# Kernel optimization log

Hardware: AMD Instinct MI355X
Metric: run time of the kernel (lower is better)

Reference implementation:

```python
import jax, jax.numpy as jnp
import numpy as np

B, H, W, D = 8, 128, 128, 256
NHEAD, DK = 8, 32
WS = 8
NH, NW = H // WS, W // WS
SHIFT = WS // 2
SCALE = 1.0 / np.sqrt(DK)
WSQ = WS * WS


def _region_labels(h, w, ws, shift):
    lab = np.zeros((h, w), np.int32)
    cnt = 0
    for hs in (slice(0, h - ws), slice(h - ws, h - shift), slice(h - shift, h)):
        for vs in (slice(0, w - ws), slice(w - ws, w - shift), slice(w - shift, w)):
            lab[hs, vs] = cnt
            cnt += 1
    return np.roll(lab, (-shift, -shift), axis=(0, 1))


def _window_labels(lab, ws, nh, nw):
    return lab.reshape(nh, ws, nw, ws).transpose(0, 2, 1, 3).reshape(nh, nw, ws * ws)


# static Swin attention mask: (nh, nw, WSQ, WSQ) bool, True = masked
_lq = _window_labels(_region_labels(H, W, WS, SHIFT), WS, NH, NW)
_lk = _window_labels(_region_labels(H, W, WS, SHIFT), WS, NH, NW)
MASK = jnp.asarray(_lq[..., :, None] != _lk[..., None, :])

# static relative position index: (WSQ, WSQ) into (2*WS-1)^2 table
_coords = np.stack(np.meshgrid(np.arange(WS), np.arange(WS), indexing='ij'), -1).reshape(-1, 2)
_rel = _coords[:, None, :] - _coords[None, :, :] + (WS - 1)  # in [0, 2*WS-2]
REL_INDEX = jnp.asarray(_rel[..., 0] * (2 * WS - 1) + _rel[..., 1])


def _cyclic_shift(t, s):
    # t: (B, nhead, H, W, d)
    return jnp.roll(t, (-s, -s), axis=(2, 3))


def _partition(t):
    # (B, nhead, H, W, d) -> (B, nhead, NH, NW, WSQ, d)
    b, nh_, _, _, d = t.shape
    t = t.reshape(b, nh_, NH, WS, NW, WS, d)
    return t.transpose(0, 1, 2, 4, 3, 5, 6).reshape(b, nh_, NH, NW, WSQ, d)


def _merge(t):
    # (B, nhead, NH, NW, WSQ, d) -> (B, nhead, H, W, d)
    b, nh_, _, _, _, d = t.shape
    t = t.reshape(b, nh_, NH, NW, WS, WS, d).transpose(0, 1, 2, 4, 3, 5, 6)
    return t.reshape(b, nh_, NH * WS, NW * WS, d)


def setup_inputs() -> dict:
    key = jax.random.key(0)
    ks = jax.random.split(key, 6)
    return {
        'x': jax.random.normal(ks[0], (B, H, W, D), jnp.float32),
        'z': jax.random.normal(ks[1], (B, H, W, D), jnp.float32),
        'Wq': jax.random.normal(ks[2], (D, D), jnp.float32) * 0.02,
        'bq': jnp.zeros((D,), jnp.float32),
        'Wkv': jax.random.normal(ks[3], (D, 2 * D), jnp.float32) * 0.02,
        'bkv': jnp.zeros((2 * D,), jnp.float32),
        'Wo': jax.random.normal(ks[4], (D, D), jnp.float32) * 0.02,
        'bo': jnp.zeros((D,), jnp.float32),
        'rel_table': jax.random.normal(ks[5], ((2 * WS - 1) ** 2, NHEAD), jnp.float32) * 0.02,
    }


def reference(x, z, Wq, bq, Wkv, bkv, Wo, bo, rel_table):
    b = x.shape[0]
    q = (x @ Wq + bq).reshape(b, H, W, NHEAD, DK).transpose(0, 3, 1, 2, 4)
    kv = (z @ Wkv + bkv).reshape(b, H, W, 2, NHEAD, DK).transpose(3, 0, 4, 1, 2, 5)
    k, v = kv[0], kv[1]

    q = _partition(_cyclic_shift(q, SHIFT))
    k = _partition(_cyclic_shift(k, SHIFT))
    v = _partition(_cyclic_shift(v, SHIFT))

    # scores: (B, nhead, NH, NW, WSQ, WSQ)
    scores = jnp.einsum('bhijqd,bhijkd->bhijqk', q, k) * SCALE
    pe = rel_table[REL_INDEX]                       # (WSQ, WSQ, nhead)
    scores = scores + pe.transpose(2, 0, 1)[None, :, None, None]
    scores = jnp.where(MASK, jnp.float32(-1e9), scores)
    attn = jax.nn.softmax(scores, axis=-1)

    out = jnp.einsum('bhijqk,bhijkd->bhijqd', attn, v)
    out = _cyclic_shift(_merge(out), -SHIFT)        # (B, nhead, H, W, DK)
    out = out.transpose(0, 2, 3, 1, 4).reshape(b, H, W, D)
    return out @ Wo + bo
```

## Files before the change

### kernel.cpp

```cpp
#include <hip/hip_runtime.h>
#include <hip/hip_bf16.h>


typedef __bf16  bf16x8 __attribute__((ext_vector_type(8)));
typedef short   short8 __attribute__((ext_vector_type(8)));
typedef short   short4v __attribute__((ext_vector_type(4)));
typedef float   f32x4  __attribute__((ext_vector_type(4)));

#define SCALE_F 0.17677669529663687f

__device__ __forceinline__ short f2bs(float f){
    __hip_bfloat16 h = __float2bfloat16(f);
    return __builtin_bit_cast(short, h);
}
__device__ __forceinline__ short8 cvt8(float4 a, float4 b){
    short8 t;
    t[0]=f2bs(a.x); t[1]=f2bs(a.y); t[2]=f2bs(a.z); t[3]=f2bs(a.w);
    t[4]=f2bs(b.x); t[5]=f2bs(b.y); t[6]=f2bs(b.z); t[7]=f2bs(b.w);
    return t;
}
__device__ __forceinline__ int strip3(int r, int c){
    if (c == 0) return 0;
    if (c == 1) return (r < 4) ? 0 : 1;
    return (r < 4) ? 2 : 0;
}

__global__ __launch_bounds__(256) void prep_k(const float* __restrict__ Wq,
                                              const float* __restrict__ Wkv,
                                              const float* __restrict__ Wo,
                                              const float* __restrict__ rel,
                                              short* __restrict__ Wqt,
                                              short* __restrict__ Wkvt,
                                              short* __restrict__ Wot,
                                              float* __restrict__ ADD){
    int i = blockIdx.x * 256 + threadIdx.x;
    if (i < 65536){
        int n = i >> 8, k = i & 255;
        Wqt[i] = f2bs(Wq[k * 256 + n]);
    } else if (i < 196608){
        int j = i - 65536;
        int n = j >> 8, k = j & 255;
        Wkvt[j] = f2bs(Wkv[k * 512 + n]);
    } else if (i < 262144){
        int j = i - 196608;
        int n = j >> 8, k = j & 255;
        Wot[j] = f2bs(Wo[k * 256 + n]);
    } else {
        int j = i - 262144;
        int k = j & 63, q = (j >> 6) & 63, head = (j >> 12) & 7, cls = j >> 15;
        int wiC = cls / 3, wjC = cls - wiC * 3;
        int qr = q >> 3, qc = q & 7, kr = k >> 3, kc = k & 7;
        int lq = strip3(qr, wiC) * 3 + strip3(qc, wjC);
        int lk = strip3(kr, wiC) * 3 + strip3(kc, wjC);
        float pe = rel[((qr - kr + 7) * 15 + (qc - kc + 7)) * 8 + head];
        ADD[j] = (lq != lk) ? -1e9f : pe;
    }
}

__global__ __launch_bounds__(512, 2) void qkv_k(
    const float* __restrict__ x, const float* __restrict__ z,
    const short* __restrict__ Wqt, const short* __restrict__ Wkvt,
    const float* __restrict__ bq, const float* __restrict__ bkv,
    short* __restrict__ Qw, short* __restrict__ Kw, short* __restrict__ Vw){
    __shared__ __align__(16) short lds[2 * 16896];
    const int tid = threadIdx.x, w = tid >> 6, lane = tid & 63;
    const int l15 = lane & 15, g = lane >> 4;
    const int bx = blockIdx.x;
    const int wj = bx & 15, wi = (bx >> 4) & 15, b = bx >> 8;
    const f32x4 zero = {0.f,0.f,0.f,0.f};

#pragma unroll
    for (int i=0;i<4;++i){
        const int u = tid + i*512;
        const int p = u >> 5, c8 = u & 31;
        const int pr = ((wi << 3) + (p >> 3) + 4) & 127;
        const int pc = ((wj << 3) + (p & 7) + 4) & 127;
        const size_t gidx = ((((((size_t)b << 7) | pr) << 7) | pc) << 8) + c8*8;
        const float4* xp = reinterpret_cast<const float4*>(x + gidx);
        float4 a0 = xp[0], a1 = xp[1];
        *reinterpret_cast<short8*>(lds + p*264 + c8*8) = cvt8(a0, a1);
        const float4* zp = reinterpret_cast<const float4*>(z + gidx);
        float4 b0 = zp[0], b1 = zp[1];
        *reinterpret_cast<short8*>(lds + 16896 + p*264 + c8*8) = cvt8(b0, b1);
    }
    __syncthreads();

    const int c0 = w * 32;
    const size_t base = ((((size_t)b*8 + w)*16 + wi)*16 + wj) * 2048;

    {
        f32x4 acc[4][2];
#pragma unroll
        for (int mi=0;mi<4;++mi){ acc[mi][0]=zero; acc[mi][1]=zero; }
#pragma unroll
        for (int kt=0;kt<8;++kt){
            bf16x8 af[4], wf[2];
#pragma unroll
            for (int nj=0;nj<2;++nj)
                wf[nj] = *reinterpret_cast<const bf16x8*>(Wqt + (size_t)(c0 + nj*16 + l15)*256 + kt*32 + g*8);
#pragma unroll
            for (int mi=0;mi<4;++mi)
                af[mi] = *reinterpret_cast<const bf16x8*>(lds + (mi*16 + l15)*264 + kt*32 + g*8);
#pragma unroll
            for (int mi=0;mi<4;++mi)
#pragma unroll
                for (int nj=0;nj<2;++nj)
                    acc[mi][nj] = __builtin_amdgcn_mfma_f32_16x16x32_bf16(af[mi], wf[nj], acc[mi][nj], 0,0,0);
        }
#pragma unroll
        for (int nj=0;nj<2;++nj){
            float bv = bq[c0 + nj*16 + l15];
#pragma unroll
            for (int mi=0;mi<4;++mi)
#pragma unroll
                for (int r=0;r<4;++r)
                    Qw[base + (size_t)(mi*16 + g*4 + r)*32 + nj*16 + l15] = f2bs(acc[mi][nj][r] + bv);
        }
    }
    {
        f32x4 acc[4][2];
#pragma unroll
        for (int mi=0;mi<4;++mi){ acc[mi][0]=zero; acc[mi][1]=zero; }
#pragma unroll
        for (int kt=0;kt<8;++kt){
            bf16x8 af[4], wf[2];
#pragma unroll
            for (int nj=0;nj<2;++nj)
                wf[nj] = *reinterpret_cast<const bf16x8*>(Wkvt + (size_t)(c0 + nj*16 + l15)*256 + kt*32 + g*8);
#pragma unroll
            for (int mi=0;mi<4;++mi)
                af[mi] = *reinterpret_cast<const bf16x8*>(lds + 16896 + (mi*16 + l15)*264 + kt*32 + g*8);
#pragma unroll
            for (int mi=0;mi<4;++mi)
#pragma unroll
                for (int nj=0;nj<2;++nj)
                    acc[mi][nj] = __builtin_amdgcn_mfma_f32_16x16x32_bf16(af[mi], wf[nj], acc[mi][nj], 0,0,0);
        }
#pragma unroll
        for (int nj=0;nj<2;++nj){
            float bv = bkv[c0 + nj*16 + l15];
#pragma unroll
            for (int mi=0;mi<4;++mi)
#pragma unroll
                for (int r=0;r<4;++r)
                    Kw[base + (size_t)(mi*16 + g*4 + r)*32 + nj*16 + l15] = f2bs(acc[mi][nj][r] + bv);
        }
    }
    {
        f32x4 acc[4][2];
#pragma unroll
        for (int mi=0;mi<4;++mi){ acc[mi][0]=zero; acc[mi][1]=zero; }
#pragma unroll
        for (int kt=0;kt<8;++kt){
            bf16x8 af[4], wf[2];
#pragma unroll
            for (int nj=0;nj<2;++nj)
                wf[nj] = *reinterpret_cast<const bf16x8*>(Wkvt + (size_t)(256 + c0 + nj*16 + l15)*256 + kt*32 + g*8);
#pragma unroll
            for (int mi=0;mi<4;++mi)
                af[mi] = *reinterpret_cast<const bf16x8*>(lds + 16896 + (mi*16 + l15)*264 + kt*32 + g*8);
#pragma unroll
            for (int mi=0;mi<4;++mi)
#pragma unroll
                for (int nj=0;nj<2;++nj)
                    acc[mi][nj] = __builtin_amdgcn_mfma_f32_16x16x32_bf16(af[mi], wf[nj], acc[mi][nj], 0,0,0);
        }
#pragma unroll
        for (int nj=0;nj<2;++nj){
            float bv = bkv[256 + c0 + nj*16 + l15];
            const int dk = nj*16 + l15;
#pragma unroll
            for (int mi=0;mi<4;++mi){
                short4v t;
#pragma unroll
                for (int r=0;r<4;++r) t[r] = f2bs(acc[mi][nj][r] + bv);
                *reinterpret_cast<short4v*>(Vw + base + (size_t)dk*64 + mi*16 + g*4) = t;
            }
        }
    }
}

__global__ __launch_bounds__(256, 2) void attnO_k(
    const short* __restrict__ Qw, const short* __restrict__ Kw,
    const short* __restrict__ Vw, const short* __restrict__ Wot,
    const float* __restrict__ bo, const float* __restrict__ ADD,
    float* __restrict__ out){
    __shared__ __align__(16) short lds[4*4608 + 16896];
    const int tid = threadIdx.x, w = tid >> 6, lane = tid & 63;
    const int l15 = lane & 15, g = lane >> 4;
    const int bx = blockIdx.x;
    const int wj = bx & 15, wi = (bx >> 4) & 15, b = bx >> 8;
    const int wiC = (wi > 13) ? wi - 13 : 0;
    const int wjC = (wj > 13) ? wj - 13 : 0;
    short* P   = lds + w * 4608;
    short* att = lds + 18432;
    const f32x4 zero = {0.f,0.f,0.f,0.f};

    for (int hh = 0; hh < 2; ++hh){
        const int h = w + hh * 4;
        const size_t base = ((((size_t)b*8 + h)*16 + wi)*16 + wj) * 2048;

        bf16x8 aq[4], bk[4];
#pragma unroll
        for (int mi=0;mi<4;++mi)
            aq[mi] = *reinterpret_cast<const bf16x8*>(Qw + base + (size_t)(mi*16 + l15)*32 + g*8);
#pragma unroll
        for (int ni=0;ni<4;++ni)
            bk[ni] = *reinterpret_cast<const bf16x8*>(Kw + base + (size_t)(ni*16 + l15)*32 + g*8);
        f32x4 s[4][4];
#pragma unroll
        for (int mi=0;mi<4;++mi)
#pragma unroll
            for (int ni=0;ni<4;++ni)
                s[mi][ni] = __builtin_amdgcn_mfma_f32_16x16x32_bf16(aq[mi], bk[ni], zero, 0,0,0);

        const float* addb = ADD + (size_t)(((wiC*3 + wjC)*8 + h) << 12);
        float rs[4][4];
#pragma unroll
        for (int mi=0;mi<4;++mi){
            const int qbase = mi*16 + g*4;
#pragma unroll
            for (int ni=0;ni<4;++ni){
                const int k = ni*16 + l15;
#pragma unroll
                for (int r=0;r<4;++r)
                    s[mi][ni][r] = fmaf(s[mi][ni][r], SCALE_F, addb[((qbase + r) << 6) + k]);
            }
#pragma unroll
            for (int r=0;r<4;++r){
                float mx = fmaxf(fmaxf(s[mi][0][r], s[mi][1][r]), fmaxf(s[mi][2][r], s[mi][3][r]));
                mx = fmaxf(mx, __shfl_xor(mx, 1));
                mx = fmaxf(mx, __shfl_xor(mx, 2));
                mx = fmaxf(mx, __shfl_xor(mx, 4));
                mx = fmaxf(mx, __shfl_xor(mx, 8));
                float sum = 0.f;
#pragma unroll
                for (int ni=0;ni<4;++ni){
                    float p = __expf(s[mi][ni][r] - mx);
                    s[mi][ni][r] = p;
                    sum += p;
                }
                sum += __shfl_xor(sum, 1);
                sum += __shfl_xor(sum, 2);
                sum += __shfl_xor(sum, 4);
                sum += __shfl_xor(sum, 8);
                rs[mi][r] = 1.f / sum;
                const int q = qbase + r;
#pragma unroll
                for (int ni=0;ni<4;++ni)
                    P[q*72 + ni*16 + l15] = f2bs(s[mi][ni][r]);
            }
        }

        f32x4 o[4][2];
#pragma unroll
        for (int mi=0;mi<4;++mi){ o[mi][0]=zero; o[mi][1]=zero; }
#pragma unroll
        for (int ks=0;ks<2;++ks){
            bf16x8 pa[4], vb[2];
#pragma unroll
            for (int mi=0;mi<4;++mi)
                pa[mi] = *reinterpret_cast<const bf16x8*>(P + (mi*16 + l15)*72 + ks*32 + g*8);
#pragma unroll
            for (int nj=0;nj<2;++nj)
                vb[nj] = *reinterpret_cast<const bf16x8*>(Vw + base + (size_t)(nj*16 + l15)*64 + ks*32 + g*8);
#pragma unroll
            for (int mi=0;mi<4;++mi)
#pragma unroll
                for (int nj=0;nj<2;++nj)
                    o[mi][nj] = __builtin_amdgcn_mfma_f32_16x16x32_bf16(pa[mi], vb[nj], o[mi][nj], 0,0,0);
        }

#pragma unroll
        for (int mi=0;mi<4;++mi)
#pragma unroll
            for (int nj=0;nj<2;++nj)
#pragma unroll
                for (int r=0;r<4;++r)
                    att[(mi*16 + g*4 + r)*264 + h*32 + nj*16 + l15] = f2bs(o[mi][nj][r] * rs[mi][r]);
    }
    __syncthreads();

    f32x4 acc[4][4];
#pragma unroll
    for (int mi=0;mi<4;++mi)
#pragma unroll
        for (int nj=0;nj<4;++nj) acc[mi][nj] = zero;
#pragma unroll
    for (int kt=0;kt<8;++kt){
        bf16x8 af[4], bfm[4];
#pragma unroll
        for (int mi=0;mi<4;++mi)
            af[mi] = *reinterpret_cast<const bf16x8*>(att + (mi*16 + l15)*264 + kt*32 + g*8);
#pragma unroll
        for (int nj=0;nj<4;++nj)
            bfm[nj] = *reinterpret_cast<const bf16x8*>(Wot + (size_t)(w*64 + nj*16 + l15)*256 + kt*32 + g*8);
#pragma unroll
        for (int mi=0;mi<4;++mi)
#pragma unroll
            for (int nj=0;nj<4;++nj)
                acc[mi][nj] = __builtin_amdgcn_mfma_f32_16x16x32_bf16(af[mi], bfm[nj], acc[mi][nj], 0,0,0);
    }
#pragma unroll
    for (int nj=0;nj<4;++nj){
        const int col = w*64 + nj*16 + l15;
        const float bv = bo[col];
#pragma unroll
        for (int mi=0;mi<4;++mi)
#pragma unroll
            for (int r=0;r<4;++r){
                const int p = mi*16 + g*4 + r;
                const int pr = ((wi << 3) + (p >> 3) + 4) & 127;
                const int pc = ((wj << 3) + (p & 7) + 4) & 127;
                const size_t gp = ((((size_t)b << 7) | pr) << 7) | pc;
                out[gp * 256 + col] = acc[mi][nj][r] + bv;
            }
    }
}

extern "C" void kernel_launch(void* const* d_in, const int* in_sizes, int n_in,
                              void* d_out, int out_size, void* d_ws, size_t ws_size,
                              hipStream_t stream) {
    const float* x    = (const float*)d_in[0];
    const float* z    = (const float*)d_in[1];
    const float* Wq   = (const float*)d_in[2];
    const float* bq   = (const float*)d_in[3];
    const float* Wkv  = (const float*)d_in[4];
    const float* bkv  = (const float*)d_in[5];
    const float* Wo   = (const float*)d_in[6];
    const float* bo   = (const float*)d_in[7];
    const float* rel  = (const float*)d_in[8];

    char* ws = (char*)d_ws;
    short* Wqt  = (short*)(ws);
    short* Wkvt = (short*)(ws + 131072);
    short* Wot  = (short*)(ws + 393216);
    float* ADD  = (float*)(ws + 524288);
    short* Qw   = (short*)(ws + 2097152);
    short* Kw   = (short*)(ws + 69206016);
    short* Vw   = (short*)(ws + 136314880);

    prep_k <<<2176, 256, 0, stream>>>(Wq, Wkv, Wo, rel, Wqt, Wkvt, Wot, ADD);
    qkv_k  <<<2048, 512, 0, stream>>>(x, z, Wqt, Wkvt, bq, bkv, Qw, Kw, Vw);
    attnO_k<<<2048, 256, 0, stream>>>(Qw, Kw, Vw, Wot, bo, ADD, (float*)d_out);
}
```

Before: 274.1 us.

## Split QKV projection into separate Q and KV blocks with halved LDS

The QKV projection kernel now launches twice as many blocks: one half loads only x and computes Q, the other loads only z and computes K and V. Each block stages a single input tile in LDS, halving shared memory per block, and the launch-bounds occupancy hint is raised from 2 to 8. The intent is more resident blocks and better latency hiding for the global loads. The trade-off is imbalanced blocks (KV blocks do twice the MFMA work of Q blocks) and more total blocks. The attention kernel's LDS array size is also rewritten as a literal with the same value.

Result: slower. 817.0 us (+198.1%).

```diff
diff --git a/kernel.cpp b/kernel.cpp
--- a/kernel.cpp
+++ b/kernel.cpp
@@ -57,17 +57,64 @@
     }
 }
 
-__global__ __launch_bounds__(512, 2) void qkv_k(
+template<bool VT>
+__device__ __forceinline__ void proj_g(const short* __restrict__ As,
+                                       const short* __restrict__ Wt, int c0,
+                                       const float* __restrict__ bias,
+                                       short* __restrict__ dst, int l15, int g){
+    f32x4 acc[4][2];
+    const f32x4 zero = {0.f,0.f,0.f,0.f};
+#pragma unroll
+    for (int mi=0;mi<4;++mi){ acc[mi][0]=zero; acc[mi][1]=zero; }
+#pragma unroll
+    for (int kt=0;kt<8;++kt){
+        bf16x8 af[4], wf[2];
+#pragma unroll
+        for (int nj=0;nj<2;++nj)
+            wf[nj] = *reinterpret_cast<const bf16x8*>(Wt + (size_t)(c0 + nj*16 + l15)*256 + kt*32 + g*8);
+#pragma unroll
+        for (int mi=0;mi<4;++mi)
+            af[mi] = *reinterpret_cast<const bf16x8*>(As + (mi*16 + l15)*264 + kt*32 + g*8);
+#pragma unroll
+        for (int mi=0;mi<4;++mi)
+#pragma unroll
+            for (int nj=0;nj<2;++nj)
+                acc[mi][nj] = __builtin_amdgcn_mfma_f32_16x16x32_bf16(af[mi], wf[nj], acc[mi][nj], 0,0,0);
+    }
+#pragma unroll
+    for (int nj=0;nj<2;++nj){
+        float bv = bias[c0 + nj*16 + l15];
+        if (VT){
+            const int dk = nj*16 + l15;
+#pragma unroll
+            for (int mi=0;mi<4;++mi){
+                short4v t;
+#pragma unroll
+                for (int r=0;r<4;++r) t[r] = f2bs(acc[mi][nj][r] + bv);
+                *reinterpret_cast<short4v*>(dst + (size_t)dk*64 + mi*16 + g*4) = t;
+            }
+        } else {
+#pragma unroll
+            for (int mi=0;mi<4;++mi)
+#pragma unroll
+                for (int r=0;r<4;++r)
+                    dst[(size_t)(mi*16 + g*4 + r)*32 + nj*16 + l15] = f2bs(acc[mi][nj][r] + bv);
+        }
+    }
+}
+
+__global__ __launch_bounds__(512, 8) void qkv_k(
     const float* __restrict__ x, const float* __restrict__ z,
     const short* __restrict__ Wqt, const short* __restrict__ Wkvt,
     const float* __restrict__ bq, const float* __restrict__ bkv,
     short* __restrict__ Qw, short* __restrict__ Kw, short* __restrict__ Vw){
-    __shared__ __align__(16) short lds[2 * 16896];
+    __shared__ __align__(16) short lds[16896];
     const int tid = threadIdx.x, w = tid >> 6, lane = tid & 63;
     const int l15 = lane & 15, g = lane >> 4;
     const int bx = blockIdx.x;
-    const int wj = bx & 15, wi = (bx >> 4) & 15, b = bx >> 8;
-    const f32x4 zero = {0.f,0.f,0.f,0.f};
+    const int seg = bx >> 11, win = bx & 2047;
+    const int wj = win & 15, wi = (win >> 4) & 15, b = win >> 8;
+    const float* __restrict__ src = seg ? z : x;
 
 #pragma unroll
     for (int i=0;i<4;++i){
@@ -76,107 +123,19 @@
         const int pr = ((wi << 3) + (p >> 3) + 4) & 127;
         const int pc = ((wj << 3) + (p & 7) + 4) & 127;
         const size_t gidx = ((((((size_t)b << 7) | pr) << 7) | pc) << 8) + c8*8;
-        const float4* xp = reinterpret_cast<const float4*>(x + gidx);
-        float4 a0 = xp[0], a1 = xp[1];
+        const float4* sp = reinterpret_cast<const float4*>(src + gidx);
+        float4 a0 = sp[0], a1 = sp[1];
         *reinterpret_cast<short8*>(lds + p*264 + c8*8) = cvt8(a0, a1);
-        const float4* zp = reinterpret_cast<const float4*>(z + gidx);
-        float4 b0 = zp[0], b1 = zp[1];
-        *reinterpret_cast<short8*>(lds + 16896 + p*264 + c8*8) = cvt8(b0, b1);
     }
     __syncthreads();
 
     const int c0 = w * 32;
     const size_t base = ((((size_t)b*8 + w)*16 + wi)*16 + wj) * 2048;
-
-    {
-        f32x4 acc[4][2];
-#pragma unroll
-        for (int mi=0;mi<4;++mi){ acc[mi][0]=zero; acc[mi][1]=zero; }
-#pragma unroll
-        for (int kt=0;kt<8;++kt){
-            bf16x8 af[4], wf[2];
-#pragma unroll
-            for (int nj=0;nj<2;++nj)
-                wf[nj] = *reinterpret_cast<const bf16x8*>(Wqt + (size_t)(c0 + nj*16 + l15)*256 + kt*32 + g*8);
-#pragma unroll
-            for (int mi=0;mi<4;++mi)
-                af[mi] = *reinterpret_cast<const bf16x8*>(lds + (mi*16 + l15)*264 + kt*32 + g*8);
-#pragma unroll
-            for (int mi=0;mi<4;++mi)
-#pragma unroll
-                for (int nj=0;nj<2;++nj)
-                    acc[mi][nj] = __builtin_amdgcn_mfma_f32_16x16x32_bf16(af[mi], wf[nj], acc[mi][nj], 0,0,0);
-        }
-#pragma unroll
-        for (int nj=0;nj<2;++nj){
-            float bv = bq[c0 + nj*16 + l15];
-#pragma unroll
-            for (int mi=0;mi<4;++mi)
-#pragma unroll
-                for (int r=0;r<4;++r)
-                    Qw[base + (size_t)(mi*16 + g*4 + r)*32 + nj*16 + l15] = f2bs(acc[mi][nj][r] + bv);
-        }
-    }
-    {
-        f32x4 acc[4][2];
-#pragma unroll
-        for (int mi=0;mi<4;++mi){ acc[mi][0]=zero; acc[mi][1]=zero; }
-#pragma unroll
-        for (int kt=0;kt<8;++kt){
-            bf16x8 af[4], wf[2];
-#pragma unroll
-            for (int nj=0;nj<2;++nj)
-                wf[nj] = *reinterpret_cast<const bf16x8*>(Wkvt + (size_t)(c0 + nj*16 + l15)*256 + kt*32 + g*8);
-#pragma unroll
-            for (int mi=0;mi<4;++mi)
-                af[mi] = *reinterpret_cast<const bf16x8*>(lds + 16896 + (mi*16 + l15)*264 + kt*32 + g*8);
-#pragma unroll
-            for (int mi=0;mi<4;++mi)
-#pragma unroll
-                for (int nj=0;nj<2;++nj)
-                    acc[mi][nj] = __builtin_amdgcn_mfma_f32_16x16x32_bf16(af[mi], wf[nj], acc[mi][nj], 0,0,0);
-        }
-#pragma unroll
-        for (int nj=0;nj<2;++nj){
-            float bv = bkv[c0 + nj*16 + l15];
-#pragma unroll
-            for (int mi=0;mi<4;++mi)
-#pragma unroll
-                for (int r=0;r<4;++r)
-                    Kw[base + (size_t)(mi*16 + g*4 + r)*32 + nj*16 + l15] = f2bs(acc[mi][nj][r] + bv);
-        }
-    }
-    {
-        f32x4 acc[4][2];
-#pragma unroll
-        for (int mi=0;mi<4;++mi){ acc[mi][0]=zero; acc[mi][1]=zero; }
-#pragma unroll
-        for (int kt=0;kt<8;++kt){
-            bf16x8 af[4], wf[2];
-#pragma unroll
-            for (int nj=0;nj<2;++nj)
-                wf[nj] = *reinterpret_cast<const bf16x8*>(Wkvt + (size_t)(256 + c0 + nj*16 + l15)*256 + kt*32 + g*8);
-#pragma unroll
-            for (int mi=0;mi<4;++mi)
-                af[mi] = *reinterpret_cast<const bf16x8*>(lds + 16896 + (mi*16 + l15)*264 + kt*32 + g*8);
-#pragma unroll
-            for (int mi=0;mi<4;++mi)
-#pragma unroll
-                for (int nj=0;nj<2;++nj)
-                    acc[mi][nj] = __builtin_amdgcn_mfma_f32_16x16x32_bf16(af[mi], wf[nj], acc[mi][nj], 0,0,0);
-        }
-#pragma unroll
-        for (int nj=0;nj<2;++nj){
-            float bv = bkv[256 + c0 + nj*16 + l15];
-            const int dk = nj*16 + l15;
-#pragma unroll
-            for (int mi=0;mi<4;++mi){
-                short4v t;
-#pragma unroll
-                for (int r=0;r<4;++r) t[r] = f2bs(acc[mi][nj][r] + bv);
-                *reinterpret_cast<short4v*>(Vw + base + (size_t)dk*64 + mi*16 + g*4) = t;
-            }
-        }
+    if (seg == 0){
+        proj_g<false>(lds, Wqt, c0, bq, Qw + base, l15, g);
+    } else {
+        proj_g<false>(lds, Wkvt, c0,       bkv, Kw + base, l15, g);
+        proj_g<true >(lds, Wkvt, 256 + c0, bkv, Vw + base, l15, g);
     }
 }
 
@@ -185,7 +144,7 @@
     const short* __restrict__ Vw, const short* __restrict__ Wot,
     const float* __restrict__ bo, const float* __restrict__ ADD,
     float* __restrict__ out){
-    __shared__ __align__(16) short lds[4*4608 + 16896];
+    __shared__ __align__(16) short lds[35328];
     const int tid = threadIdx.x, w = tid >> 6, lane = tid & 63;
     const int l15 = lane & 15, g = lane >> 4;
     const int bx = blockIdx.x;
@@ -341,6 +300,6 @@
     short* Vw   = (short*)(ws + 136314880);
 
     prep_k <<<2176, 256, 0, stream>>>(Wq, Wkv, Wo, rel, Wqt, Wkvt, Wot, ADD);
-    qkv_k  <<<2048, 512, 0, stream>>>(x, z, Wqt, Wkvt, bq, bkv, Qw, Kw, Vw);
+    qkv_k  <<<4096, 512, 0, stream>>>(x, z, Wqt, Wkvt, bq, bkv, Qw, Kw, Vw);
     attnO_k<<<2048, 256, 0, stream>>>(Qw, Kw, Vw, Wot, bo, ADD, (float*)d_out);
 }
```

## Split QKV projection into separate x and z blocks with LDS-staged coalesced stores

Applied to the files above, without the earlier changes.

The QKV kernel now runs twice as many blocks: one set projects x to Q and the other projects z to K and V. Each block stages only one input tile in shared memory, which halves LDS use and lets launch bounds ask for more resident blocks. K and V are computed in a single fused loop that shares the A fragments. Outputs are staged through LDS and then written as coalesced 8-byte vectors instead of scattered 2-byte stores. The attnO LDS array is resized, apparently by the same number of bytes. The cost is extra barriers, more register pressure in the fused K/V loop, and the x and z blocks doing unequal amounts of work.

Measured after the change: 276.4 us. Within noise of the previous version (+0.9%).

```diff
diff --git a/kernel.cpp b/kernel.cpp
--- a/kernel.cpp
+++ b/kernel.cpp
@@ -57,16 +57,18 @@
     }
 }
 
-__global__ __launch_bounds__(512, 2) void qkv_k(
+__global__ __launch_bounds__(512, 4) void qkv_k(
     const float* __restrict__ x, const float* __restrict__ z,
     const short* __restrict__ Wqt, const short* __restrict__ Wkvt,
     const float* __restrict__ bq, const float* __restrict__ bkv,
     short* __restrict__ Qw, short* __restrict__ Kw, short* __restrict__ Vw){
-    __shared__ __align__(16) short lds[2 * 16896];
+    __shared__ __align__(16) short lds[18432];
     const int tid = threadIdx.x, w = tid >> 6, lane = tid & 63;
     const int l15 = lane & 15, g = lane >> 4;
     const int bx = blockIdx.x;
-    const int wj = bx & 15, wi = (bx >> 4) & 15, b = bx >> 8;
+    const int seg = bx >> 11, win = bx & 2047;
+    const int wj = win & 15, wi = (win >> 4) & 15, b = win >> 8;
+    const float* __restrict__ src = seg ? z : x;
     const f32x4 zero = {0.f,0.f,0.f,0.f};
 
 #pragma unroll
@@ -76,19 +78,16 @@
         const int pr = ((wi << 3) + (p >> 3) + 4) & 127;
         const int pc = ((wj << 3) + (p & 7) + 4) & 127;
         const size_t gidx = ((((((size_t)b << 7) | pr) << 7) | pc) << 8) + c8*8;
-        const float4* xp = reinterpret_cast<const float4*>(x + gidx);
-        float4 a0 = xp[0], a1 = xp[1];
+        const float4* sp = reinterpret_cast<const float4*>(src + gidx);
+        float4 a0 = sp[0], a1 = sp[1];
         *reinterpret_cast<short8*>(lds + p*264 + c8*8) = cvt8(a0, a1);
-        const float4* zp = reinterpret_cast<const float4*>(z + gidx);
-        float4 b0 = zp[0], b1 = zp[1];
-        *reinterpret_cast<short8*>(lds + 16896 + p*264 + c8*8) = cvt8(b0, b1);
     }
     __syncthreads();
 
     const int c0 = w * 32;
-    const size_t base = ((((size_t)b*8 + w)*16 + wi)*16 + wj) * 2048;
-
-    {
+    const size_t winoff = ((size_t)wi*16 + wj) * 2048;
+
+    if (seg == 0){
         f32x4 acc[4][2];
 #pragma unroll
         for (int mi=0;mi<4;++mi){ acc[mi][0]=zero; acc[mi][1]=zero; }
@@ -107,6 +106,7 @@
                 for (int nj=0;nj<2;++nj)
                     acc[mi][nj] = __builtin_amdgcn_mfma_f32_16x16x32_bf16(af[mi], wf[nj], acc[mi][nj], 0,0,0);
         }
+        __syncthreads();
 #pragma unroll
         for (int nj=0;nj<2;++nj){
             float bv = bq[c0 + nj*16 + l15];
@@ -114,28 +114,43 @@
             for (int mi=0;mi<4;++mi)
 #pragma unroll
                 for (int r=0;r<4;++r)
-                    Qw[base + (size_t)(mi*16 + g*4 + r)*32 + nj*16 + l15] = f2bs(acc[mi][nj][r] + bv);
-        }
-    }
-    {
-        f32x4 acc[4][2];
-#pragma unroll
-        for (int mi=0;mi<4;++mi){ acc[mi][0]=zero; acc[mi][1]=zero; }
+                    lds[w*2304 + (mi*16 + g*4 + r)*36 + nj*16 + l15] = f2bs(acc[mi][nj][r] + bv);
+        }
+        __syncthreads();
+        const int off = tid*4, p = off >> 5, c = off & 31;
+#pragma unroll
+        for (int hw=0; hw<8; ++hw){
+            const size_t dstb = ((size_t)b*8 + hw)*524288 + winoff;
+            *reinterpret_cast<short4v*>(Qw + dstb + off) =
+                *reinterpret_cast<const short4v*>(lds + hw*2304 + p*36 + c);
+        }
+    } else {
+        f32x4 accK[4][2], accV[4][2];
+#pragma unroll
+        for (int mi=0;mi<4;++mi){
+            accK[mi][0]=zero; accK[mi][1]=zero;
+            accV[mi][0]=zero; accV[mi][1]=zero;
+        }
 #pragma unroll
         for (int kt=0;kt<8;++kt){
-            bf16x8 af[4], wf[2];
-#pragma unroll
-            for (int nj=0;nj<2;++nj)
-                wf[nj] = *reinterpret_cast<const bf16x8*>(Wkvt + (size_t)(c0 + nj*16 + l15)*256 + kt*32 + g*8);
-#pragma unroll
-            for (int mi=0;mi<4;++mi)
-                af[mi] = *reinterpret_cast<const bf16x8*>(lds + 16896 + (mi*16 + l15)*264 + kt*32 + g*8);
-#pragma unroll
-            for (int mi=0;mi<4;++mi)
-#pragma unroll
-                for (int nj=0;nj<2;++nj)
-                    acc[mi][nj] = __builtin_amdgcn_mfma_f32_16x16x32_bf16(af[mi], wf[nj], acc[mi][nj], 0,0,0);
-        }
+            bf16x8 af[4], wfK[2], wfV[2];
+#pragma unroll
+            for (int nj=0;nj<2;++nj){
+                wfK[nj] = *reinterpret_cast<const bf16x8*>(Wkvt + (size_t)(c0 + nj*16 + l15)*256 + kt*32 + g*8);
+                wfV[nj] = *reinterpret_cast<const bf16x8*>(Wkvt + (size_t)(256 + c0 + nj*16 + l15)*256 + kt*32 + g*8);
+            }
+#pragma unroll
+            for (int mi=0;mi<4;++mi)
+                af[mi] = *reinterpret_cast<const bf16x8*>(lds + (mi*16 + l15)*264 + kt*32 + g*8);
+#pragma unroll
+            for (int mi=0;mi<4;++mi)
+#pragma unroll
+                for (int nj=0;nj<2;++nj){
+                    accK[mi][nj] = __builtin_amdgcn_mfma_f32_16x16x32_bf16(af[mi], wfK[nj], accK[mi][nj], 0,0,0);
+                    accV[mi][nj] = __builtin_amdgcn_mfma_f32_16x16x32_bf16(af[mi], wfV[nj], accV[mi][nj], 0,0,0);
+                }
+        }
+        __syncthreads();
 #pragma unroll
         for (int nj=0;nj<2;++nj){
             float bv = bkv[c0 + nj*16 + l15];
@@ -143,28 +158,19 @@
             for (int mi=0;mi<4;++mi)
 #pragma unroll
                 for (int r=0;r<4;++r)
-                    Kw[base + (size_t)(mi*16 + g*4 + r)*32 + nj*16 + l15] = f2bs(acc[mi][nj][r] + bv);
-        }
-    }
-    {
-        f32x4 acc[4][2];
-#pragma unroll
-        for (int mi=0;mi<4;++mi){ acc[mi][0]=zero; acc[mi][1]=zero; }
-#pragma unroll
-        for (int kt=0;kt<8;++kt){
-            bf16x8 af[4], wf[2];
-#pragma unroll
-            for (int nj=0;nj<2;++nj)
-                wf[nj] = *reinterpret_cast<const bf16x8*>(Wkvt + (size_t)(256 + c0 + nj*16 + l15)*256 + kt*32 + g*8);
-#pragma unroll
-            for (int mi=0;mi<4;++mi)
-                af[mi] = *reinterpret_cast<const bf16x8*>(lds + 16896 + (mi*16 + l15)*264 + kt*32 + g*8);
-#pragma unroll
-            for (int mi=0;mi<4;++mi)
-#pragma unroll
-                for (int nj=0;nj<2;++nj)
-                    acc[mi][nj] = __builtin_amdgcn_mfma_f32_16x16x32_bf16(af[mi], wf[nj], acc[mi][nj], 0,0,0);
-        }
+                    lds[w*2304 + (mi*16 + g*4 + r)*36 + nj*16 + l15] = f2bs(accK[mi][nj][r] + bv);
+        }
+        __syncthreads();
+        {
+            const int off = tid*4, p = off >> 5, c = off & 31;
+#pragma unroll
+            for (int hw=0; hw<8; ++hw){
+                const size_t dstb = ((size_t)b*8 + hw)*524288 + winoff;
+                *reinterpret_cast<short4v*>(Kw + dstb + off) =
+                    *reinterpret_cast<const short4v*>(lds + hw*2304 + p*36 + c);
+            }
+        }
+        __syncthreads();
 #pragma unroll
         for (int nj=0;nj<2;++nj){
             float bv = bkv[256 + c0 + nj*16 + l15];
@@ -173,8 +179,18 @@
             for (int mi=0;mi<4;++mi){
                 short4v t;
 #pragma unroll
-                for (int r=0;r<4;++r) t[r] = f2bs(acc[mi][nj][r] + bv);
-                *reinterpret_cast<short4v*>(Vw + base + (size_t)dk*64 + mi*16 + g*4) = t;
+                for (int r=0;r<4;++r) t[r] = f2bs(accV[mi][nj][r] + bv);
+                *reinterpret_cast<short4v*>(lds + w*2176 + dk*68 + mi*16 + g*4) = t;
+            }
+        }
+        __syncthreads();
+        {
+            const int off = tid*4, dk = off >> 6, pix = off & 63;
+#pragma unroll
+            for (int hw=0; hw<8; ++hw){
+                const size_t dstb = ((size_t)b*8 + hw)*524288 + winoff;
+                *reinterpret_cast<short4v*>(Vw + dstb + off) =
+                    *reinterpret_cast<const short4v*>(lds + hw*2176 + dk*68 + pix);
             }
         }
     }
@@ -185,7 +201,7 @@
     const short* __restrict__ Vw, const short* __restrict__ Wot,
     const float* __restrict__ bo, const float* __restrict__ ADD,
     float* __restrict__ out){
-    __shared__ __align__(16) short lds[4*4608 + 16896];
+    __shared__ __align__(16) short lds[35328];
     const int tid = threadIdx.x, w = tid >> 6, lane = tid & 63;
     const int l15 = lane & 15, g = lane >> 4;
     const int bx = blockIdx.x;
@@ -341,6 +357,6 @@
     short* Vw   = (short*)(ws + 136314880);
 
     prep_k <<<2176, 256, 0, stream>>>(Wq, Wkv, Wo, rel, Wqt, Wkvt, Wot, ADD);
-    qkv_k  <<<2048, 512, 0, stream>>>(x, z, Wqt, Wkvt, bq, bkv, Qw, Kw, Vw);
+    qkv_k  <<<4096, 512, 0, stream>>>(x, z, Wqt, Wkvt, bq, bkv, Qw, Kw, Vw);
     attnO_k<<<2048, 256, 0, stream>>>(Qw, Kw, Vw, Wot, bo, ADD, (float*)d_out);
 }
```
